# Kernel optimization log

Hardware: AMD Instinct MI355X
Metric: run time of the kernel (lower is better)

The kernel has to match this reference:

```python
import jax, jax.numpy as jnp
import numpy as np

N = 50000
E = 800000
IN_DIM = 128
HID = 32
OUT_DIM = 64
HEADS = 4
NEG_SLOPE = 0.2  # DGL GATConv default leaky_relu slope


def setup_inputs() -> dict:
    key = jax.random.key(0)
    ks = jax.random.split(key, 16)
    h = jax.random.normal(ks[0], (N, IN_DIM), dtype=jnp.float32)
    src = jax.random.randint(ks[1], (E,), 0, N, dtype=jnp.int32)
    dst = jax.random.randint(ks[2], (E,), 0, N, dtype=jnp.int32)
    s = 0.05
    # layer 1: in 128 -> heads*32 = 128
    W1 = jax.random.normal(ks[3], (IN_DIM, HEADS * HID), dtype=jnp.float32) * s
    al1 = jax.random.normal(ks[4], (HEADS, HID), dtype=jnp.float32) * s
    ar1 = jax.random.normal(ks[5], (HEADS, HID), dtype=jnp.float32) * s
    # layer 2: in 128 -> heads*32 = 128
    W2 = jax.random.normal(ks[6], (HEADS * HID, HEADS * HID), dtype=jnp.float32) * s
    al2 = jax.random.normal(ks[7], (HEADS, HID), dtype=jnp.float32) * s
    ar2 = jax.random.normal(ks[8], (HEADS, HID), dtype=jnp.float32) * s
    # last layer: in 128 -> heads*64 = 256 (needs residual projection)
    W3 = jax.random.normal(ks[9], (HEADS * HID, HEADS * OUT_DIM), dtype=jnp.float32) * s
    al3 = jax.random.normal(ks[10], (HEADS, OUT_DIM), dtype=jnp.float32) * s
    ar3 = jax.random.normal(ks[11], (HEADS, OUT_DIM), dtype=jnp.float32) * s
    resW3 = jax.random.normal(ks[12], (HEADS * HID, HEADS * OUT_DIM), dtype=jnp.float32) * s
    return {"h": h, "W1": W1, "al1": al1, "ar1": ar1, "W2": W2, "al2": al2,
            "ar2": ar2, "W3": W3, "al3": al3, "ar3": ar3, "resW3": resW3,
            "src": src, "dst": dst}


def gat_layer(h, src, dst, W, al, ar, heads, out_feats, res_W=None, act=None):
    n = h.shape[0]
    feat = (h @ W).reshape(n, heads, out_feats)          # [N,H,D]
    el = jnp.einsum('nhd,hd->nh', feat, al)               # [N,H]
    er = jnp.einsum('nhd,hd->nh', feat, ar)               # [N,H]
    e = jax.nn.leaky_relu(el[src] + er[dst], NEG_SLOPE)   # [E,H]
    m = jax.ops.segment_max(e, dst, num_segments=n)       # per-dst max, [N,H]
    ex = jnp.exp(e - m[dst])
    denom = jax.ops.segment_sum(ex, dst, num_segments=n)  # [N,H]
    alpha = ex / denom[dst]                               # edge softmax, [E,H]
    msg = feat[src] * alpha[:, :, None]                   # [E,H,D]
    rst = jax.ops.segment_sum(msg, dst, num_segments=n)   # [N,H,D]
    res = (h @ res_W) if res_W is not None else h
    rst = rst + res.reshape(n, heads, out_feats)
    if act is not None:
        rst = act(rst)
    return rst


def reference(h, W1, al1, ar1, W2, al2, ar2, W3, al3, ar3, resW3, src, dst):
    n = h.shape[0]
    x = gat_layer(h, src, dst, W1, al1, ar1, HEADS, HID, act=jax.nn.relu)
    x = x.reshape(n, -1)
    # feat_drop=0.3 on layer 2 omitted (eval/deterministic mode)
    x = gat_layer(x, src, dst, W2, al2, ar2, HEADS, HID, act=jax.nn.relu)
    x = x.reshape(n, -1)
    x = gat_layer(x, src, dst, W3, al3, ar3, HEADS, OUT_DIM, res_W=resW3)
    return x.mean(axis=1)  # mean over heads -> [N, OUT_DIM]
```

## Files before the change

### kernel.cpp

```cpp
#include <hip/hip_runtime.h>
#include <hip/hip_bf16.h>
#include <math.h>


#define NEG_SLOPE 0.2f

typedef __attribute__((ext_vector_type(8))) __bf16 bf16x8;
typedef __attribute__((ext_vector_type(4))) float f32x4;

__device__ __forceinline__ float leaky(float x) { return fmaxf(x, NEG_SLOPE * x); }
__device__ __forceinline__ ushort f2bf(float f) {
    unsigned u = __float_as_uint(f);
    return (ushort)((u + 0x7fffu + ((u >> 16) & 1u)) >> 16);
}
__device__ __forceinline__ float bf2f(ushort b) { return __uint_as_float(((unsigned)b) << 16); }
__device__ __forceinline__ float lo16f(unsigned v) { return __uint_as_float(v << 16); }
__device__ __forceinline__ float hi16f(unsigned v) { return __uint_as_float(v & 0xffff0000u); }


__global__ void hist_kernel(const int* __restrict__ dst, int* __restrict__ deg, int E) {
    int i = blockIdx.x * blockDim.x + threadIdx.x;
    if (i < E) atomicAdd(&deg[dst[i]], 1);
}

__global__ void block_scan_kernel(const int* __restrict__ deg, int* __restrict__ loc,
                                  int* __restrict__ bsum, int n) {
    __shared__ int sm[1024];
    const int tid = threadIdx.x;
    const int i = blockIdx.x * 1024 + tid;
    int v = (i < n) ? deg[i] : 0;
    sm[tid] = v;
    __syncthreads();
    for (int off = 1; off < 1024; off <<= 1) {
        int t = (tid >= off) ? sm[tid - off] : 0;
        __syncthreads();
        sm[tid] += t;
        __syncthreads();
    }
    if (i < n) loc[i] = sm[tid] - v;
    if (tid == 1023) bsum[blockIdx.x] = sm[1023];
}

__global__ void apply_scan_kernel(const int* __restrict__ loc, const int* __restrict__ bsum,
                                  int* __restrict__ row_ptr, int* __restrict__ cursor,
                                  int n, int nb) {
    __shared__ int pb[64];
    const int tid = threadIdx.x;
    if (tid < 64) {
        int v = (tid < nb) ? bsum[tid] : 0;
        int orig = v;
        for (int off = 1; off < 64; off <<= 1) {
            int t = __shfl_up(v, off);
            if (tid >= off) v += t;
        }
        pb[tid] = v - orig;
        if (tid == 63 && blockIdx.x == 0) row_ptr[n] = v;
    }
    __syncthreads();
    int i = blockIdx.x * blockDim.x + tid;
    if (i < n) {
        int v = loc[i] + pb[i >> 10];
        row_ptr[i] = v;
        cursor[i]  = v;
    }
}

__global__ void scatter_kernel(const int* __restrict__ src, const int* __restrict__ dst,
                               int* __restrict__ cursor, int* __restrict__ ssrc, int E) {
    int i = blockIdx.x * blockDim.x + threadIdx.x;
    if (i < E) {
        int s = src[i];
        int pos = atomicAdd(&cursor[dst[i]], 1);
        ssrc[pos] = s;
    }
}


__global__ void prep_kernel(const float* __restrict__ h, ushort* __restrict__ xbh,
                            const float* __restrict__ W1, ushort* __restrict__ W1th,
                            const float* __restrict__ W2, ushort* __restrict__ W2th,
                            const float* __restrict__ W3, ushort* __restrict__ W3th,
                            const float* __restrict__ rW3, ushort* __restrict__ rWmh,
                            int* __restrict__ cursor, int nh4, int n) {
    int i = blockIdx.x * blockDim.x + threadIdx.x;
    if (i < nh4) {
        float4 v = ((const float4*)h)[i];
        ushort4 o;
        o.x = f2bf(v.x); o.y = f2bf(v.y); o.z = f2bf(v.z); o.w = f2bf(v.w);
        ((ushort4*)xbh)[i] = o;
        return;
    }
    int j = i - nh4;
    if (j < 16384) {
        int c = j >> 7, k = j & 127;
        int kd = k ^ ((c & 7) << 3);
        W1th[c * 128 + kd] = f2bf(W1[k * 128 + c]);
    } else if (j < 32768) {
        j -= 16384;
        int c = j >> 7, k = j & 127;
        int kd = k ^ ((c & 7) << 3);
        W2th[c * 128 + kd] = f2bf(W2[k * 128 + c]);
    } else if (j < 65536) {
        j -= 32768;
        int c = j >> 7, k = j & 127;
        int kd = k ^ ((c & 7) << 3);
        W3th[c * 128 + kd] = f2bf(W3[k * 256 + c]);
    } else if (j < 73728) {
        j -= 65536;
        int c = j >> 7, k = j & 127;
        const float* row = rW3 + (size_t)k * 256;
        float v = 0.25f * ((row[c] + row[64 + c]) + (row[128 + c] + row[192 + c]));
        int kd = k ^ ((c & 7) << 3);
        rWmh[c * 128 + kd] = f2bf(v);
    } else if (j < 73728 + n) {
        cursor[j - 73728] = 0;
    }
}


__global__ void __launch_bounds__(256)
gemm_kernel(const ushort* __restrict__ Ah, const ushort* __restrict__ Bth,
            const ushort* __restrict__ B2th,
            ushort* __restrict__ Cb, float* __restrict__ C2f,
            const float* __restrict__ alv, const float* __restrict__ arv,
            float* __restrict__ el, float* __restrict__ er,
            int M, int Ncols, int dshift) {
    extern __shared__ ushort Ws[];
    ushort* Ws2 = Ws + 128 * 128;
    const int tid = threadIdx.x;
    const int wv = tid >> 6;
    const int lane = tid & 63;
    const int l15 = lane & 15;
    const int g = lane >> 4;
    const int bm = blockIdx.x * 128 + wv * 32;
    const int bn = blockIdx.y * 128;
    const bool do2 = (B2th != nullptr) && (blockIdx.y == 0);

    {
        const uint4* gh = (const uint4*)(Bth + (size_t)bn * 128);
        uint4* sh = (uint4*)Ws;
#pragma unroll
        for (int it = 0; it < 8; ++it) sh[it * 256 + tid] = gh[it * 256 + tid];
        if (do2) {
            const uint4* g2 = (const uint4*)B2th;
            uint4* s2 = (uint4*)Ws2;
#pragma unroll
            for (int it = 0; it < 4; ++it) s2[it * 256 + tid] = g2[it * 256 + tid];
        }
    }
    __syncthreads();

    const int m0 = bm + l15;
    const int m1 = bm + 16 + l15;
    const int mc0 = (m0 < M) ? m0 : (M - 1);
    const int mc1 = (m1 < M) ? m1 : (M - 1);
    bf16x8 xh[2][4];
#pragma unroll
    for (int kk = 0; kk < 4; ++kk) {
        xh[0][kk] = *(const bf16x8*)(Ah + (size_t)mc0 * 128 + kk * 32 + g * 8);
        xh[1][kk] = *(const bf16x8*)(Ah + (size_t)mc1 * 128 + kk * 32 + g * 8);
    }

    f32x4 acc[2][8] = {};
    f32x4 acc2[2][4] = {};
    const int swz = (l15 & 7) << 4;
#pragma unroll
    for (int n = 0; n < 8; ++n) {
        const int colb = (n * 16 + l15) * 256;
#pragma unroll
        for (int kk = 0; kk < 4; ++kk) {
            const int boff = colb + ((kk * 64 + g * 16) ^ swz);
            bf16x8 wh = *(const bf16x8*)((const char*)Ws + boff);
            acc[0][n] = __builtin_amdgcn_mfma_f32_16x16x32_bf16(wh, xh[0][kk], acc[0][n], 0, 0, 0);
            acc[1][n] = __builtin_amdgcn_mfma_f32_16x16x32_bf16(wh, xh[1][kk], acc[1][n], 0, 0, 0);
        }
    }
    if (do2) {
#pragma unroll
        for (int n = 0; n < 4; ++n) {
            const int colb = (n * 16 + l15) * 256;
#pragma unroll
            for (int kk = 0; kk < 4; ++kk) {
                const int boff = colb + ((kk * 64 + g * 16) ^ swz);
                bf16x8 w2 = *(const bf16x8*)((const char*)Ws2 + boff);
                acc2[0][n] = __builtin_amdgcn_mfma_f32_16x16x32_bf16(w2, xh[0][kk], acc2[0][n], 0, 0, 0);
                acc2[1][n] = __builtin_amdgcn_mfma_f32_16x16x32_bf16(w2, xh[1][kk], acc2[1][n], 0, 0, 0);
            }
        }
    }

#pragma unroll
    for (int mf = 0; mf < 2; ++mf) {
        const int m = (mf == 0) ? m0 : m1;
        const bool valid = (m < M);
        if (valid) {
            size_t ro = (size_t)m * Ncols;
#pragma unroll
            for (int n = 0; n < 8; ++n) {
                int col = bn + n * 16 + g * 4;
                ushort4 o;
                o.x = f2bf(acc[mf][n][0]); o.y = f2bf(acc[mf][n][1]);
                o.z = f2bf(acc[mf][n][2]); o.w = f2bf(acc[mf][n][3]);
                *(ushort4*)&Cb[ro + col] = o;
            }
            if (do2) {
#pragma unroll
                for (int n = 0; n < 4; ++n) {
                    *(float4*)&C2f[(size_t)m * 64 + n * 16 + g * 4] =
                        make_float4(acc2[mf][n][0], acc2[mf][n][1],
                                    acc2[mf][n][2], acc2[mf][n][3]);
                }
            }
        }
        if (alv) {
            float e0 = 0.f, e1 = 0.f, e2 = 0.f, e3 = 0.f;
            float r0 = 0.f, r1 = 0.f, r2 = 0.f, r3 = 0.f;
            const bool four = (dshift == 5);
#pragma unroll
            for (int n = 0; n < 8; ++n) {
                float se = 0.f, sr = 0.f;
#pragma unroll
                for (int rr = 0; rr < 4; ++rr) {
                    int col = bn + n * 16 + g * 4 + rr;
                    float c = acc[mf][n][rr];
                    se += c * alv[col];
                    sr += c * arv[col];
                }
                if (four) {
                    if (n < 2)      { e0 += se; r0 += sr; }
                    else if (n < 4) { e1 += se; r1 += sr; }
                    else if (n < 6) { e2 += se; r2 += sr; }
                    else            { e3 += se; r3 += sr; }
                } else {
                    if (n < 4)      { e0 += se; r0 += sr; }
                    else            { e1 += se; r1 += sr; }
                }
            }
            e0 += __shfl_xor(e0, 16); e0 += __shfl_xor(e0, 32);
            e1 += __shfl_xor(e1, 16); e1 += __shfl_xor(e1, 32);
            r0 += __shfl_xor(r0, 16); r0 += __shfl_xor(r0, 32);
            r1 += __shfl_xor(r1, 16); r1 += __shfl_xor(r1, 32);
            if (four) {
                e2 += __shfl_xor(e2, 16); e2 += __shfl_xor(e2, 32);
                e3 += __shfl_xor(e3, 16); e3 += __shfl_xor(e3, 32);
                r2 += __shfl_xor(r2, 16); r2 += __shfl_xor(r2, 32);
                r3 += __shfl_xor(r3, 16); r3 += __shfl_xor(r3, 32);
            }
            if (valid && g == 0) {
                if (four) {
                    el[m * 4 + 0] = e0; el[m * 4 + 1] = e1;
                    el[m * 4 + 2] = e2; el[m * 4 + 3] = e3;
                    er[m * 4 + 0] = r0; er[m * 4 + 1] = r1;
                    er[m * 4 + 2] = r2; er[m * 4 + 3] = r3;
                } else {
                    int h0 = bn >> 6;
                    el[m * 4 + h0] = e0; el[m * 4 + h0 + 1] = e1;
                    er[m * 4 + h0] = r0; er[m * 4 + h0 + 1] = r1;
                }
            }
        }
    }
}


__global__ void __launch_bounds__(256)
aggregate12_kernel(const ushort* __restrict__ featb, const float* __restrict__ el,
                   const float* __restrict__ er, const int* __restrict__ row_ptr,
                   const int* __restrict__ ssrc, const float* __restrict__ resf,
                   const ushort* __restrict__ rxh, ushort* __restrict__ xbh, int n) {
    const int wid = threadIdx.x >> 6;
    const int lane = threadIdx.x & 63;
    const int node = blockIdx.x * 4 + wid;
    if (node >= n) return;
    const int beg = row_ptr[node];
    const int end = row_ptr[node + 1];
    const int half = lane >> 5;
    const int l32 = lane & 31;
    const int hh = l32 >> 3;
    const float erh = er[node * 4 + hh];

    float ssum = 0.f, a0 = 0.f, a1 = 0.f, a2 = 0.f, a3 = 0.f;
    int p = beg;
    for (; p + 8 <= end; p += 8) {
        int s[4]; uint2 v[4]; float e[4];
#pragma unroll
        for (int j = 0; j < 4; ++j) s[j] = ssrc[p + 2 * j + half];
#pragma unroll
        for (int j = 0; j < 4; ++j) v[j] = *(const uint2*)&featb[(size_t)s[j] * 128 + l32 * 4];
#pragma unroll
        for (int j = 0; j < 4; ++j) e[j] = el[s[j] * 4 + hh];
#pragma unroll
        for (int j = 0; j < 4; ++j) {
            float w = __expf(leaky(e[j] + erh));
            ssum += w;
            a0 += w * lo16f(v[j].x);
            a1 += w * hi16f(v[j].x);
            a2 += w * lo16f(v[j].y);
            a3 += w * hi16f(v[j].y);
        }
    }
    for (; p < end; p += 2) {
        int pe = p + half;
        bool ok = pe < end;
        int s = ssrc[ok ? pe : beg];
        uint2 v = *(const uint2*)&featb[(size_t)s * 128 + l32 * 4];
        float w = ok ? __expf(leaky(el[s * 4 + hh] + erh)) : 0.f;
        ssum += w;
        a0 += w * lo16f(v.x);
        a1 += w * hi16f(v.x);
        a2 += w * lo16f(v.y);
        a3 += w * hi16f(v.y);
    }
    ssum += __shfl_xor(ssum, 32);
    a0 += __shfl_xor(a0, 32);
    a1 += __shfl_xor(a1, 32);
    a2 += __shfl_xor(a2, 32);
    a3 += __shfl_xor(a3, 32);
    float inv = (end > beg) ? 1.f / ssum : 0.f;
    if (half == 0) {
        size_t o = (size_t)node * 128 + l32 * 4;
        float rb0, rb1, rb2, rb3;
        if (resf) {
            float4 f = *(const float4*)&resf[o];
            rb0 = f.x; rb1 = f.y; rb2 = f.z; rb3 = f.w;
        } else {
            uint2 rh = *(const uint2*)&rxh[o];
            rb0 = lo16f(rh.x);
            rb1 = hi16f(rh.x);
            rb2 = lo16f(rh.y);
            rb3 = hi16f(rh.y);
        }
        float r0 = fmaxf(a0 * inv + rb0, 0.f);
        float r1 = fmaxf(a1 * inv + rb1, 0.f);
        float r2 = fmaxf(a2 * inv + rb2, 0.f);
        float r3 = fmaxf(a3 * inv + rb3, 0.f);
        uint2 oh;
        oh.x = (unsigned)f2bf(r0) | ((unsigned)f2bf(r1) << 16);
        oh.y = (unsigned)f2bf(r2) | ((unsigned)f2bf(r3) << 16);
        *(uint2*)&xbh[o] = oh;
    }
}


__global__ void __launch_bounds__(256)
aggregate3_kernel(const ushort* __restrict__ featb, const float* __restrict__ el,
                  const float* __restrict__ er, const int* __restrict__ row_ptr,
                  const int* __restrict__ ssrc, const float* __restrict__ resmean,
                  float* __restrict__ out, int n) {
    const int wid = threadIdx.x >> 6;
    const int lane = threadIdx.x & 63;
    const int node = blockIdx.x * 4 + wid;
    if (node >= n) return;
    const int beg = row_ptr[node];
    const int end = row_ptr[node + 1];
    const int half = lane >> 5;
    const int l32 = lane & 31;
    const int hh = l32 >> 3;
    const float erh = er[node * 4 + hh];

    float c[8] = {};
    float ssum = 0.f;
    int p = beg;
    for (; p + 8 <= end; p += 8) {
        int s[4]; uint4 v[4]; float e[4];
#pragma unroll
        for (int j = 0; j < 4; ++j) s[j] = ssrc[p + 2 * j + half];
#pragma unroll
        for (int j = 0; j < 4; ++j) v[j] = *(const uint4*)&featb[(size_t)s[j] * 256 + l32 * 8];
#pragma unroll
        for (int j = 0; j < 4; ++j) e[j] = el[s[j] * 4 + hh];
#pragma unroll
        for (int j = 0; j < 4; ++j) {
            float w = __expf(leaky(e[j] + erh));
            ssum += w;
            c[0] += w * lo16f(v[j].x); c[1] += w * hi16f(v[j].x);
            c[2] += w * lo16f(v[j].y); c[3] += w * hi16f(v[j].y);
            c[4] += w * lo16f(v[j].z); c[5] += w * hi16f(v[j].z);
            c[6] += w * lo16f(v[j].w); c[7] += w * hi16f(v[j].w);
        }
    }
    for (; p < end; p += 2) {
        int pe = p + half;
        bool ok = pe < end;
        int s = ssrc[ok ? pe : beg];
        uint4 v = *(const uint4*)&featb[(size_t)s * 256 + l32 * 8];
        float w = ok ? __expf(leaky(el[s * 4 + hh] + erh)) : 0.f;
        ssum += w;
        c[0] += w * lo16f(v.x); c[1] += w * hi16f(v.x);
        c[2] += w * lo16f(v.y); c[3] += w * hi16f(v.y);
        c[4] += w * lo16f(v.z); c[5] += w * hi16f(v.z);
        c[6] += w * lo16f(v.w); c[7] += w * hi16f(v.w);
    }
    ssum += __shfl_xor(ssum, 32);
#pragma unroll
    for (int i = 0; i < 8; ++i) c[i] += __shfl_xor(c[i], 32);
    float inv = (end > beg) ? 1.f / ssum : 0.f;
#pragma unroll
    for (int i = 0; i < 8; ++i) c[i] *= inv;
#pragma unroll
    for (int i = 0; i < 8; ++i) c[i] += __shfl_xor(c[i], 8);
#pragma unroll
    for (int i = 0; i < 8; ++i) c[i] += __shfl_xor(c[i], 16);
    if (lane < 8) {
        const int d0 = lane * 8;
        float4 rm0 = *(const float4*)&resmean[(size_t)node * 64 + d0];
        float4 rm1 = *(const float4*)&resmean[(size_t)node * 64 + d0 + 4];
        *(float4*)&out[(size_t)node * 64 + d0] =
            make_float4(0.25f * c[0] + rm0.x, 0.25f * c[1] + rm0.y,
                        0.25f * c[2] + rm0.z, 0.25f * c[3] + rm0.w);
        *(float4*)&out[(size_t)node * 64 + d0 + 4] =
            make_float4(0.25f * c[4] + rm1.x, 0.25f * c[5] + rm1.y,
                        0.25f * c[6] + rm1.z, 0.25f * c[7] + rm1.w);
    }
}


extern "C" void kernel_launch(void* const* d_in, const int* in_sizes, int n_in,
                              void* d_out, int out_size, void* d_ws, size_t ws_size,
                              hipStream_t stream) {
    const float* h   = (const float*)d_in[0];
    const float* W1  = (const float*)d_in[1];
    const float* al1 = (const float*)d_in[2];
    const float* ar1 = (const float*)d_in[3];
    const float* W2  = (const float*)d_in[4];
    const float* al2 = (const float*)d_in[5];
    const float* ar2 = (const float*)d_in[6];
    const float* W3  = (const float*)d_in[7];
    const float* al3 = (const float*)d_in[8];
    const float* ar3 = (const float*)d_in[9];
    const float* rW3 = (const float*)d_in[10];
    const int* src   = (const int*)d_in[11];
    const int* dstv  = (const int*)d_in[12];
    const int N = in_sizes[0] / 128;
    const int E = in_sizes[11];
    float* out = (float*)d_out;

    char* p = (char*)d_ws;
    auto alloc = [&](size_t bytes) -> char* {
        char* q = p;
        p += (bytes + 255) & ~(size_t)255;
        return q;
    };
    int*    row_ptr = (int*)alloc((size_t)(N + 1) * 4);
    int*    cursor  = (int*)alloc((size_t)N * 4);
    int*    loc     = (int*)alloc((size_t)N * 4);
    int*    bsum    = (int*)alloc(64 * 4);
    int*    ssrc    = (int*)alloc((size_t)E * 4);
    float*  el      = (float*)alloc((size_t)N * 16);
    float*  er      = (float*)alloc((size_t)N * 16);
    ushort* featb   = (ushort*)alloc((size_t)N * 256 * 2);
    ushort* xbh     = (ushort*)alloc((size_t)N * 128 * 2);
    ushort* W1th = (ushort*)alloc(128 * 128 * 2);
    ushort* W2th = (ushort*)alloc(128 * 128 * 2);
    ushort* W3th = (ushort*)alloc(256 * 128 * 2);
    ushort* rWmh = (ushort*)alloc(64 * 128 * 2);
    float*  resmean = (float*)alloc((size_t)N * 64 * 4);

    const int nh4 = N * 32;
    const int prep_total = nh4 + 73728 + N;
    prep_kernel<<<(prep_total + 255) / 256, 256, 0, stream>>>(
        h, xbh, W1, W1th, W2, W2th, W3, W3th, rW3, rWmh, cursor, nh4, N);

    hist_kernel<<<(E + 255) / 256, 256, 0, stream>>>(dstv, cursor, E);
    int nb = (N + 1023) / 1024;
    block_scan_kernel<<<nb, 1024, 0, stream>>>(cursor, loc, bsum, N);
    apply_scan_kernel<<<(N + 255) / 256, 256, 0, stream>>>(loc, bsum, row_ptr, cursor, N, nb);
    scatter_kernel<<<(E + 255) / 256, 256, 0, stream>>>(src, dstv, cursor, ssrc, E);

    const int gx = (N + 127) / 128;
    dim3 g1(gx, 1);
    dim3 g3(gx, 2);
    int agg_grid = (N + 3) / 4;
    const size_t lds1 = 128 * 128 * sizeof(ushort);
    const size_t lds3 = (128 * 128 + 64 * 128) * sizeof(ushort);

    gemm_kernel<<<g1, 256, lds1, stream>>>(xbh, W1th, nullptr, featb, nullptr,
                                           al1, ar1, el, er, N, 128, 5);
    aggregate12_kernel<<<agg_grid, 256, 0, stream>>>(featb, el, er, row_ptr, ssrc,
                                                     h, nullptr, xbh, N);

    gemm_kernel<<<g1, 256, lds1, stream>>>(xbh, W2th, nullptr, featb, nullptr,
                                           al2, ar2, el, er, N, 128, 5);
    aggregate12_kernel<<<agg_grid, 256, 0, stream>>>(featb, el, er, row_ptr, ssrc,
                                                     nullptr, xbh, xbh, N);

    gemm_kernel<<<g3, 256, lds3, stream>>>(xbh, W3th, rWmh, featb, resmean,
                                           al3, ar3, el, er, N, 256, 6);
    aggregate3_kernel<<<agg_grid, 256, 0, stream>>>(featb, el, er, row_ptr, ssrc, resmean, out, N);
}
```

Measured before the change: 383.0 us.

## Reorder layer-3 GAT to aggregate inputs before projecting with W3

Layer 3 no longer computes the 256-wide projected features. It folds al3/ar3 into W3 so attention logits come straight from a small 80-column GEMM along with the residual mean. The aggregation then gathers the 128-wide bf16 input per head into a 512-wide per-node buffer, and a final GEMM against a head-mean W3 projects it and adds the residual. This halves per-edge gather bytes in the heaviest aggregation, at the cost of an extra kernel, a 512-wide intermediate buffer and bf16 rounding of the folded weights.

```diff
diff --git a/kernel.cpp b/kernel.cpp
--- a/kernel.cpp
+++ b/kernel.cpp
@@ -79,8 +79,9 @@
 __global__ void prep_kernel(const float* __restrict__ h, ushort* __restrict__ xbh,
                             const float* __restrict__ W1, ushort* __restrict__ W1th,
                             const float* __restrict__ W2, ushort* __restrict__ W2th,
-                            const float* __restrict__ W3, ushort* __restrict__ W3th,
-                            const float* __restrict__ rW3, ushort* __restrict__ rWmh,
+                            const float* __restrict__ W3, ushort* __restrict__ Bpre,
+                            ushort* __restrict__ Wft, const float* __restrict__ rW3,
+                            const float* __restrict__ al3, const float* __restrict__ ar3,
                             int* __restrict__ cursor, int nh4, int n) {
     int i = blockIdx.x * blockDim.x + threadIdx.x;
     if (i < nh4) {
@@ -100,53 +101,59 @@
         int c = j >> 7, k = j & 127;
         int kd = k ^ ((c & 7) << 3);
         W2th[c * 128 + kd] = f2bf(W2[k * 128 + c]);
-    } else if (j < 65536) {
+    } else if (j < 40960) {
         j -= 32768;
-        int c = j >> 7, k = j & 127;
-        int kd = k ^ ((c & 7) << 3);
-        W3th[c * 128 + kd] = f2bf(W3[k * 256 + c]);
-    } else if (j < 73728) {
-        j -= 65536;
         int c = j >> 7, k = j & 127;
         const float* row = rW3 + (size_t)k * 256;
         float v = 0.25f * ((row[c] + row[64 + c]) + (row[128 + c] + row[192 + c]));
         int kd = k ^ ((c & 7) << 3);
-        rWmh[c * 128 + kd] = f2bf(v);
-    } else if (j < 73728 + n) {
-        cursor[j - 73728] = 0;
+        Bpre[c * 128 + kd] = f2bf(v);
+    } else if (j < 41984) {
+        j -= 40960;
+        int c2 = j >> 7, k = j & 127;
+        int hh = c2 & 3;
+        const float* vec = (c2 < 4) ? al3 : ar3;
+        const float* wrow = W3 + (size_t)k * 256 + hh * 64;
+        const float* vrow = vec + hh * 64;
+        float s = 0.f;
+        for (int d = 0; d < 64; ++d) s += wrow[d] * vrow[d];
+        int c = 64 + c2;
+        int kd = k ^ ((c & 7) << 3);
+        Bpre[c * 128 + kd] = f2bf(s);
+    } else if (j < 43008) {
+        j -= 41984;
+        Bpre[72 * 128 + j] = 0;
+    } else if (j < 75776) {
+        j -= 43008;
+        int c = j >> 9, k = j & 511;
+        int hh = k >> 7, d = k & 127;
+        float v = 0.25f * W3[(size_t)d * 256 + hh * 64 + c];
+        int kd = k ^ ((c & 7) << 3);
+        Wft[c * 512 + kd] = f2bf(v);
+    } else if (j < 75776 + n) {
+        cursor[j - 75776] = 0;
     }
 }
 
 
 __global__ void __launch_bounds__(256)
 gemm_kernel(const ushort* __restrict__ Ah, const ushort* __restrict__ Bth,
-            const ushort* __restrict__ B2th,
-            ushort* __restrict__ Cb, float* __restrict__ C2f,
+            ushort* __restrict__ Cb,
             const float* __restrict__ alv, const float* __restrict__ arv,
-            float* __restrict__ el, float* __restrict__ er,
-            int M, int Ncols, int dshift) {
-    extern __shared__ ushort Ws[];
-    ushort* Ws2 = Ws + 128 * 128;
+            float* __restrict__ el, float* __restrict__ er, int M) {
+    __shared__ ushort Ws[128 * 128];
     const int tid = threadIdx.x;
     const int wv = tid >> 6;
     const int lane = tid & 63;
     const int l15 = lane & 15;
     const int g = lane >> 4;
     const int bm = blockIdx.x * 128 + wv * 32;
-    const int bn = blockIdx.y * 128;
-    const bool do2 = (B2th != nullptr) && (blockIdx.y == 0);
 
     {
-        const uint4* gh = (const uint4*)(Bth + (size_t)bn * 128);
+        const uint4* gh = (const uint4*)Bth;
         uint4* sh = (uint4*)Ws;
 #pragma unroll
         for (int it = 0; it < 8; ++it) sh[it * 256 + tid] = gh[it * 256 + tid];
-        if (do2) {
-            const uint4* g2 = (const uint4*)B2th;
-            uint4* s2 = (uint4*)Ws2;
-#pragma unroll
-            for (int it = 0; it < 4; ++it) s2[it * 256 + tid] = g2[it * 256 + tid];
-        }
     }
     __syncthreads();
 
@@ -162,7 +169,6 @@
     }
 
     f32x4 acc[2][8] = {};
-    f32x4 acc2[2][4] = {};
     const int swz = (l15 & 7) << 4;
 #pragma unroll
     for (int n = 0; n < 8; ++n) {
@@ -175,89 +181,117 @@
             acc[1][n] = __builtin_amdgcn_mfma_f32_16x16x32_bf16(wh, xh[1][kk], acc[1][n], 0, 0, 0);
         }
     }
-    if (do2) {
-#pragma unroll
-        for (int n = 0; n < 4; ++n) {
-            const int colb = (n * 16 + l15) * 256;
-#pragma unroll
-            for (int kk = 0; kk < 4; ++kk) {
-                const int boff = colb + ((kk * 64 + g * 16) ^ swz);
-                bf16x8 w2 = *(const bf16x8*)((const char*)Ws2 + boff);
-                acc2[0][n] = __builtin_amdgcn_mfma_f32_16x16x32_bf16(w2, xh[0][kk], acc2[0][n], 0, 0, 0);
-                acc2[1][n] = __builtin_amdgcn_mfma_f32_16x16x32_bf16(w2, xh[1][kk], acc2[1][n], 0, 0, 0);
-            }
-        }
-    }
 
 #pragma unroll
     for (int mf = 0; mf < 2; ++mf) {
         const int m = (mf == 0) ? m0 : m1;
         const bool valid = (m < M);
         if (valid) {
-            size_t ro = (size_t)m * Ncols;
+            size_t ro = (size_t)m * 128;
 #pragma unroll
             for (int n = 0; n < 8; ++n) {
-                int col = bn + n * 16 + g * 4;
+                int col = n * 16 + g * 4;
                 ushort4 o;
                 o.x = f2bf(acc[mf][n][0]); o.y = f2bf(acc[mf][n][1]);
                 o.z = f2bf(acc[mf][n][2]); o.w = f2bf(acc[mf][n][3]);
                 *(ushort4*)&Cb[ro + col] = o;
             }
-            if (do2) {
-#pragma unroll
-                for (int n = 0; n < 4; ++n) {
-                    *(float4*)&C2f[(size_t)m * 64 + n * 16 + g * 4] =
-                        make_float4(acc2[mf][n][0], acc2[mf][n][1],
-                                    acc2[mf][n][2], acc2[mf][n][3]);
-                }
+        }
+        float e0 = 0.f, e1 = 0.f, e2 = 0.f, e3 = 0.f;
+        float r0 = 0.f, r1 = 0.f, r2 = 0.f, r3 = 0.f;
+#pragma unroll
+        for (int n = 0; n < 8; ++n) {
+            float se = 0.f, sr = 0.f;
+#pragma unroll
+            for (int rr = 0; rr < 4; ++rr) {
+                int col = n * 16 + g * 4 + rr;
+                float c = acc[mf][n][rr];
+                se += c * alv[col];
+                sr += c * arv[col];
             }
-        }
-        if (alv) {
-            float e0 = 0.f, e1 = 0.f, e2 = 0.f, e3 = 0.f;
-            float r0 = 0.f, r1 = 0.f, r2 = 0.f, r3 = 0.f;
-            const bool four = (dshift == 5);
-#pragma unroll
-            for (int n = 0; n < 8; ++n) {
-                float se = 0.f, sr = 0.f;
-#pragma unroll
-                for (int rr = 0; rr < 4; ++rr) {
-                    int col = bn + n * 16 + g * 4 + rr;
-                    float c = acc[mf][n][rr];
-                    se += c * alv[col];
-                    sr += c * arv[col];
-                }
-                if (four) {
-                    if (n < 2)      { e0 += se; r0 += sr; }
-                    else if (n < 4) { e1 += se; r1 += sr; }
-                    else if (n < 6) { e2 += se; r2 += sr; }
-                    else            { e3 += se; r3 += sr; }
-                } else {
-                    if (n < 4)      { e0 += se; r0 += sr; }
-                    else            { e1 += se; r1 += sr; }
-                }
-            }
-            e0 += __shfl_xor(e0, 16); e0 += __shfl_xor(e0, 32);
-            e1 += __shfl_xor(e1, 16); e1 += __shfl_xor(e1, 32);
-            r0 += __shfl_xor(r0, 16); r0 += __shfl_xor(r0, 32);
-            r1 += __shfl_xor(r1, 16); r1 += __shfl_xor(r1, 32);
-            if (four) {
-                e2 += __shfl_xor(e2, 16); e2 += __shfl_xor(e2, 32);
-                e3 += __shfl_xor(e3, 16); e3 += __shfl_xor(e3, 32);
-                r2 += __shfl_xor(r2, 16); r2 += __shfl_xor(r2, 32);
-                r3 += __shfl_xor(r3, 16); r3 += __shfl_xor(r3, 32);
-            }
-            if (valid && g == 0) {
-                if (four) {
-                    el[m * 4 + 0] = e0; el[m * 4 + 1] = e1;
-                    el[m * 4 + 2] = e2; el[m * 4 + 3] = e3;
-                    er[m * 4 + 0] = r0; er[m * 4 + 1] = r1;
-                    er[m * 4 + 2] = r2; er[m * 4 + 3] = r3;
-                } else {
-                    int h0 = bn >> 6;
-                    el[m * 4 + h0] = e0; el[m * 4 + h0 + 1] = e1;
-                    er[m * 4 + h0] = r0; er[m * 4 + h0 + 1] = r1;
-                }
-            }
+            if (n < 2)      { e0 += se; r0 += sr; }
+            else if (n < 4) { e1 += se; r1 += sr; }
+            else if (n < 6) { e2 += se; r2 += sr; }
+            else            { e3 += se; r3 += sr; }
+        }
+        e0 += __shfl_xor(e0, 16); e0 += __shfl_xor(e0, 32);
+        e1 += __shfl_xor(e1, 16); e1 += __shfl_xor(e1, 32);
+        e2 += __shfl_xor(e2, 16); e2 += __shfl_xor(e2, 32);
+        e3 += __shfl_xor(e3, 16); e3 += __shfl_xor(e3, 32);
+        r0 += __shfl_xor(r0, 16); r0 += __shfl_xor(r0, 32);
+        r1 += __shfl_xor(r1, 16); r1 += __shfl_xor(r1, 32);
+        r2 += __shfl_xor(r2, 16); r2 += __shfl_xor(r2, 32);
+        r3 += __shfl_xor(r3, 16); r3 += __shfl_xor(r3, 32);
+        if (valid && g == 0) {
+            el[m * 4 + 0] = e0; el[m * 4 + 1] = e1;
+            el[m * 4 + 2] = e2; el[m * 4 + 3] = e3;
+            er[m * 4 + 0] = r0; er[m * 4 + 1] = r1;
+            er[m * 4 + 2] = r2; er[m * 4 + 3] = r3;
+        }
+    }
+}
+
+
+__global__ void __launch_bounds__(256)
+pre3_kernel(const ushort* __restrict__ Ah, const ushort* __restrict__ Bpre,
+            float* __restrict__ resmean, float* __restrict__ el,
+            float* __restrict__ er, int M) {
+    __shared__ ushort Ws[80 * 128];
+    const int tid = threadIdx.x;
+    const int wv = tid >> 6;
+    const int lane = tid & 63;
+    const int l15 = lane & 15;
+    const int g = lane >> 4;
+    const int bm = blockIdx.x * 128 + wv * 32;
+
+    {
+        const uint4* gh = (const uint4*)Bpre;
+        uint4* sh = (uint4*)Ws;
+#pragma unroll
+        for (int it = 0; it < 5; ++it) sh[it * 256 + tid] = gh[it * 256 + tid];
+    }
+    __syncthreads();
+
+    const int m0 = bm + l15;
+    const int m1 = bm + 16 + l15;
+    const int mc0 = (m0 < M) ? m0 : (M - 1);
+    const int mc1 = (m1 < M) ? m1 : (M - 1);
+    bf16x8 xh[2][4];
+#pragma unroll
+    for (int kk = 0; kk < 4; ++kk) {
+        xh[0][kk] = *(const bf16x8*)(Ah + (size_t)mc0 * 128 + kk * 32 + g * 8);
+        xh[1][kk] = *(const bf16x8*)(Ah + (size_t)mc1 * 128 + kk * 32 + g * 8);
+    }
+
+    f32x4 acc[2][5] = {};
+    const int swz = (l15 & 7) << 4;
+#pragma unroll
+    for (int n = 0; n < 5; ++n) {
+        const int colb = (n * 16 + l15) * 256;
+#pragma unroll
+        for (int kk = 0; kk < 4; ++kk) {
+            const int boff = colb + ((kk * 64 + g * 16) ^ swz);
+            bf16x8 wh = *(const bf16x8*)((const char*)Ws + boff);
+            acc[0][n] = __builtin_amdgcn_mfma_f32_16x16x32_bf16(wh, xh[0][kk], acc[0][n], 0, 0, 0);
+            acc[1][n] = __builtin_amdgcn_mfma_f32_16x16x32_bf16(wh, xh[1][kk], acc[1][n], 0, 0, 0);
+        }
+    }
+
+#pragma unroll
+    for (int mf = 0; mf < 2; ++mf) {
+        const int m = (mf == 0) ? m0 : m1;
+        if (m >= M) continue;
+#pragma unroll
+        for (int n = 0; n < 4; ++n) {
+            *(float4*)&resmean[(size_t)m * 64 + n * 16 + g * 4] =
+                make_float4(acc[mf][n][0], acc[mf][n][1], acc[mf][n][2], acc[mf][n][3]);
+        }
+        if (g == 0) {
+#pragma unroll
+            for (int r = 0; r < 4; ++r) el[m * 4 + r] = acc[mf][4][r];
+        } else if (g == 1) {
+#pragma unroll
+            for (int r = 0; r < 4; ++r) er[m * 4 + r] = acc[mf][4][r];
         }
     }
 }
@@ -343,10 +377,9 @@
 
 
 __global__ void __launch_bounds__(256)
-aggregate3_kernel(const ushort* __restrict__ featb, const float* __restrict__ el,
+aggregate3_kernel(const ushort* __restrict__ xb, const float* __restrict__ el,
                   const float* __restrict__ er, const int* __restrict__ row_ptr,
-                  const int* __restrict__ ssrc, const float* __restrict__ resmean,
-                  float* __restrict__ out, int n) {
+                  const int* __restrict__ ssrc, ushort* __restrict__ aggv, int n) {
     const int wid = threadIdx.x >> 6;
     const int lane = threadIdx.x & 63;
     const int node = blockIdx.x * 4 + wid;
@@ -355,62 +388,135 @@
     const int end = row_ptr[node + 1];
     const int half = lane >> 5;
     const int l32 = lane & 31;
-    const int hh = l32 >> 3;
-    const float erh = er[node * 4 + hh];
-
-    float c[8] = {};
-    float ssum = 0.f;
+    const int hsel = l32 & 3;
+    const float erh = er[node * 4 + hsel];
+    const int wbase = half << 5;
+
+    float acc[4][4] = {};
+    float ssuml = 0.f;
     int p = beg;
     for (; p + 8 <= end; p += 8) {
-        int s[4]; uint4 v[4]; float e[4];
+        int s[4]; uint2 v[4];
 #pragma unroll
         for (int j = 0; j < 4; ++j) s[j] = ssrc[p + 2 * j + half];
 #pragma unroll
-        for (int j = 0; j < 4; ++j) v[j] = *(const uint4*)&featb[(size_t)s[j] * 256 + l32 * 8];
-#pragma unroll
-        for (int j = 0; j < 4; ++j) e[j] = el[s[j] * 4 + hh];
+        for (int j = 0; j < 4; ++j) v[j] = *(const uint2*)&xb[(size_t)s[j] * 128 + l32 * 4];
 #pragma unroll
         for (int j = 0; j < 4; ++j) {
-            float w = __expf(leaky(e[j] + erh));
-            ssum += w;
-            c[0] += w * lo16f(v[j].x); c[1] += w * hi16f(v[j].x);
-            c[2] += w * lo16f(v[j].y); c[3] += w * hi16f(v[j].y);
-            c[4] += w * lo16f(v[j].z); c[5] += w * hi16f(v[j].z);
-            c[6] += w * lo16f(v[j].w); c[7] += w * hi16f(v[j].w);
+            float ww = (l32 < 4) ? __expf(leaky(el[s[j] * 4 + hsel] + erh)) : 0.f;
+            ssuml += ww;
+            float w0 = __shfl(ww, wbase + 0);
+            float w1 = __shfl(ww, wbase + 1);
+            float w2 = __shfl(ww, wbase + 2);
+            float w3 = __shfl(ww, wbase + 3);
+            float x0 = lo16f(v[j].x), x1 = hi16f(v[j].x);
+            float x2 = lo16f(v[j].y), x3 = hi16f(v[j].y);
+            acc[0][0] += w0 * x0; acc[0][1] += w0 * x1; acc[0][2] += w0 * x2; acc[0][3] += w0 * x3;
+            acc[1][0] += w1 * x0; acc[1][1] += w1 * x1; acc[1][2] += w1 * x2; acc[1][3] += w1 * x3;
+            acc[2][0] += w2 * x0; acc[2][1] += w2 * x1; acc[2][2] += w2 * x2; acc[2][3] += w2 * x3;
+            acc[3][0] += w3 * x0; acc[3][1] += w3 * x1; acc[3][2] += w3 * x2; acc[3][3] += w3 * x3;
         }
     }
     for (; p < end; p += 2) {
         int pe = p + half;
         bool ok = pe < end;
         int s = ssrc[ok ? pe : beg];
-        uint4 v = *(const uint4*)&featb[(size_t)s * 256 + l32 * 8];
-        float w = ok ? __expf(leaky(el[s * 4 + hh] + erh)) : 0.f;
-        ssum += w;
-        c[0] += w * lo16f(v.x); c[1] += w * hi16f(v.x);
-        c[2] += w * lo16f(v.y); c[3] += w * hi16f(v.y);
-        c[4] += w * lo16f(v.z); c[5] += w * hi16f(v.z);
-        c[6] += w * lo16f(v.w); c[7] += w * hi16f(v.w);
-    }
-    ssum += __shfl_xor(ssum, 32);
-#pragma unroll
-    for (int i = 0; i < 8; ++i) c[i] += __shfl_xor(c[i], 32);
-    float inv = (end > beg) ? 1.f / ssum : 0.f;
-#pragma unroll
-    for (int i = 0; i < 8; ++i) c[i] *= inv;
-#pragma unroll
-    for (int i = 0; i < 8; ++i) c[i] += __shfl_xor(c[i], 8);
-#pragma unroll
-    for (int i = 0; i < 8; ++i) c[i] += __shfl_xor(c[i], 16);
-    if (lane < 8) {
-        const int d0 = lane * 8;
-        float4 rm0 = *(const float4*)&resmean[(size_t)node * 64 + d0];
-        float4 rm1 = *(const float4*)&resmean[(size_t)node * 64 + d0 + 4];
-        *(float4*)&out[(size_t)node * 64 + d0] =
-            make_float4(0.25f * c[0] + rm0.x, 0.25f * c[1] + rm0.y,
-                        0.25f * c[2] + rm0.z, 0.25f * c[3] + rm0.w);
-        *(float4*)&out[(size_t)node * 64 + d0 + 4] =
-            make_float4(0.25f * c[4] + rm1.x, 0.25f * c[5] + rm1.y,
-                        0.25f * c[6] + rm1.z, 0.25f * c[7] + rm1.w);
+        uint2 v = *(const uint2*)&xb[(size_t)s * 128 + l32 * 4];
+        float ww = (ok && l32 < 4) ? __expf(leaky(el[s * 4 + hsel] + erh)) : 0.f;
+        ssuml += ww;
+        float w0 = __shfl(ww, wbase + 0);
+        float w1 = __shfl(ww, wbase + 1);
+        float w2 = __shfl(ww, wbase + 2);
+        float w3 = __shfl(ww, wbase + 3);
+        if (!ok) { w0 = w1 = w2 = w3 = 0.f; }
+        float x0 = lo16f(v.x), x1 = hi16f(v.x);
+        float x2 = lo16f(v.y), x3 = hi16f(v.y);
+        acc[0][0] += w0 * x0; acc[0][1] += w0 * x1; acc[0][2] += w0 * x2; acc[0][3] += w0 * x3;
+        acc[1][0] += w1 * x0; acc[1][1] += w1 * x1; acc[1][2] += w1 * x2; acc[1][3] += w1 * x3;
+        acc[2][0] += w2 * x0; acc[2][1] += w2 * x1; acc[2][2] += w2 * x2; acc[2][3] += w2 * x3;
+        acc[3][0] += w3 * x0; acc[3][1] += w3 * x1; acc[3][2] += w3 * x2; acc[3][3] += w3 * x3;
+    }
+#pragma unroll
+    for (int hh = 0; hh < 4; ++hh)
+#pragma unroll
+        for (int d = 0; d < 4; ++d) acc[hh][d] += __shfl_xor(acc[hh][d], 32);
+    float s0 = __shfl(ssuml, 0) + __shfl(ssuml, 32);
+    float s1 = __shfl(ssuml, 1) + __shfl(ssuml, 33);
+    float s2 = __shfl(ssuml, 2) + __shfl(ssuml, 34);
+    float s3 = __shfl(ssuml, 3) + __shfl(ssuml, 35);
+    if (half == 0) {
+        const bool has = (end > beg);
+        float i0 = has ? 1.f / s0 : 0.f;
+        float i1 = has ? 1.f / s1 : 0.f;
+        float i2 = has ? 1.f / s2 : 0.f;
+        float i3 = has ? 1.f / s3 : 0.f;
+        float iv[4] = { i0, i1, i2, i3 };
+        size_t base = (size_t)node * 512 + l32 * 4;
+#pragma unroll
+        for (int hh = 0; hh < 4; ++hh) {
+            float r0 = acc[hh][0] * iv[hh];
+            float r1 = acc[hh][1] * iv[hh];
+            float r2 = acc[hh][2] * iv[hh];
+            float r3 = acc[hh][3] * iv[hh];
+            uint2 o;
+            o.x = (unsigned)f2bf(r0) | ((unsigned)f2bf(r1) << 16);
+            o.y = (unsigned)f2bf(r2) | ((unsigned)f2bf(r3) << 16);
+            *(uint2*)&aggv[base + hh * 128] = o;
+        }
+    }
+}
+
+
+__global__ void __launch_bounds__(256)
+fin_kernel(const ushort* __restrict__ aggv, const ushort* __restrict__ Wft,
+           const float* __restrict__ resmean, float* __restrict__ out, int M) {
+    __shared__ ushort Ws[64 * 512];
+    const int tid = threadIdx.x;
+    const int wv = tid >> 6;
+    const int lane = tid & 63;
+    const int l15 = lane & 15;
+    const int g = lane >> 4;
+    const int bm = blockIdx.x * 128 + wv * 32;
+
+    {
+        const uint4* gh = (const uint4*)Wft;
+        uint4* sh = (uint4*)Ws;
+#pragma unroll
+        for (int it = 0; it < 16; ++it) sh[it * 256 + tid] = gh[it * 256 + tid];
+    }
+    __syncthreads();
+
+    const int m0 = bm + l15;
+    const int m1 = bm + 16 + l15;
+    const int mc0 = (m0 < M) ? m0 : (M - 1);
+    const int mc1 = (m1 < M) ? m1 : (M - 1);
+
+    f32x4 acc[2][4] = {};
+    const int swz = (l15 & 7) << 4;
+#pragma unroll
+    for (int kk = 0; kk < 16; ++kk) {
+        bf16x8 x0 = *(const bf16x8*)(aggv + (size_t)mc0 * 512 + kk * 32 + g * 8);
+        bf16x8 x1 = *(const bf16x8*)(aggv + (size_t)mc1 * 512 + kk * 32 + g * 8);
+#pragma unroll
+        for (int n = 0; n < 4; ++n) {
+            const int boff = (n * 16 + l15) * 1024 + ((kk * 64 + g * 16) ^ swz);
+            bf16x8 wh = *(const bf16x8*)((const char*)Ws + boff);
+            acc[0][n] = __builtin_amdgcn_mfma_f32_16x16x32_bf16(wh, x0, acc[0][n], 0, 0, 0);
+            acc[1][n] = __builtin_amdgcn_mfma_f32_16x16x32_bf16(wh, x1, acc[1][n], 0, 0, 0);
+        }
+    }
+
+#pragma unroll
+    for (int mf = 0; mf < 2; ++mf) {
+        const int m = (mf == 0) ? m0 : m1;
+        if (m >= M) continue;
+#pragma unroll
+        for (int n = 0; n < 4; ++n) {
+            float4 rm = *(const float4*)&resmean[(size_t)m * 64 + n * 16 + g * 4];
+            *(float4*)&out[(size_t)m * 64 + n * 16 + g * 4] =
+                make_float4(acc[mf][n][0] + rm.x, acc[mf][n][1] + rm.y,
+                            acc[mf][n][2] + rm.z, acc[mf][n][3] + rm.w);
+        }
     }
 }
 
@@ -448,18 +554,19 @@
     int*    ssrc    = (int*)alloc((size_t)E * 4);
     float*  el      = (float*)alloc((size_t)N * 16);
     float*  er      = (float*)alloc((size_t)N * 16);
-    ushort* featb   = (ushort*)alloc((size_t)N * 256 * 2);
+    ushort* featb   = (ushort*)alloc((size_t)N * 128 * 2);
     ushort* xbh     = (ushort*)alloc((size_t)N * 128 * 2);
+    ushort* aggv    = (ushort*)alloc((size_t)N * 512 * 2);
     ushort* W1th = (ushort*)alloc(128 * 128 * 2);
     ushort* W2th = (ushort*)alloc(128 * 128 * 2);
-    ushort* W3th = (ushort*)alloc(256 * 128 * 2);
-    ushort* rWmh = (ushort*)alloc(64 * 128 * 2);
+    ushort* Bpre = (ushort*)alloc(80 * 128 * 2);
+    ushort* Wft  = (ushort*)alloc(64 * 512 * 2);
     float*  resmean = (float*)alloc((size_t)N * 64 * 4);
 
     const int nh4 = N * 32;
-    const int prep_total = nh4 + 73728 + N;
+    const int prep_total = nh4 + 75776 + N;
     prep_kernel<<<(prep_total + 255) / 256, 256, 0, stream>>>(
-        h, xbh, W1, W1th, W2, W2th, W3, W3th, rW3, rWmh, cursor, nh4, N);
+        h, xbh, W1, W1th, W2, W2th, W3, Bpre, Wft, rW3, al3, ar3, cursor, nh4, N);
 
     hist_kernel<<<(E + 255) / 256, 256, 0, stream>>>(dstv, cursor, E);
     int nb = (N + 1023) / 1024;
@@ -468,23 +575,17 @@
     scatter_kernel<<<(E + 255) / 256, 256, 0, stream>>>(src, dstv, cursor, ssrc, E);
 
     const int gx = (N + 127) / 128;
-    dim3 g1(gx, 1);
-    dim3 g3(gx, 2);
     int agg_grid = (N + 3) / 4;
-    const size_t lds1 = 128 * 128 * sizeof(ushort);
-    const size_t lds3 = (128 * 128 + 64 * 128) * sizeof(ushort);
-
-    gemm_kernel<<<g1, 256, lds1, stream>>>(xbh, W1th, nullptr, featb, nullptr,
-                                           al1, ar1, el, er, N, 128, 5);
+
+    gemm_kernel<<<gx, 256, 0, stream>>>(xbh, W1th, featb, al1, ar1, el, er, N);
     aggregate12_kernel<<<agg_grid, 256, 0, stream>>>(featb, el, er, row_ptr, ssrc,
                                                      h, nullptr, xbh, N);
 
-    gemm_kernel<<<g1, 256, lds1, stream>>>(xbh, W2th, nullptr, featb, nullptr,
-                                           al2, ar2, el, er, N, 128, 5);
+    gemm_kernel<<<gx, 256, 0, stream>>>(xbh, W2th, featb, al2, ar2, el, er, N);
     aggregate12_kernel<<<agg_grid, 256, 0, stream>>>(featb, el, er, row_ptr, ssrc,
                                                      nullptr, xbh, xbh, N);
 
-    gemm_kernel<<<g3, 256, lds3, stream>>>(xbh, W3th, rWmh, featb, resmean,
-                                           al3, ar3, el, er, N, 256, 6);
-    aggregate3_kernel<<<agg_grid, 256, 0, stream>>>(featb, el, er, row_ptr, ssrc, resmean, out, N);
-}
+    pre3_kernel<<<gx, 256, 0, stream>>>(xbh, Bpre, resmean, el, er, N);
+    aggregate3_kernel<<<agg_grid, 256, 0, stream>>>(xbh, el, er, row_ptr, ssrc, aggv, N);
+    fin_kernel<<<gx, 256, 0, stream>>>(aggv, Wft, resmean, out, N);
+}
```

Result: faster. 373.9 us (-2.4%).
